# Optimization experiments

Hardware: AMD Instinct MI355X
Metric: run time of the kernel (lower is better)

## Reference

```python
import jax, jax.numpy as jnp
import numpy as np

N = 1_000_000   # total nodes (variable + check)
V = 600_000     # variable nodes (mask = first V nodes)
H = 128         # hidden_dim


def setup_inputs() -> dict:
    key = jax.random.key(0)
    k0, k1, k2, k3 = jax.random.split(key, 4)
    node_features = jax.random.normal(k0, (N, H), dtype=jnp.float32)
    original_llr = jax.random.normal(k1, (V,), dtype=jnp.float32)
    # canonical layout: variable nodes occupy the first V slots
    var_node_mask = jnp.arange(N) < V
    # llr_proj: Linear(1, H)
    W_llr = jax.random.normal(k2, (1, H), dtype=jnp.float32) * 0.1
    b_llr = jnp.zeros((H,), dtype=jnp.float32)
    # gate: Linear(2H, H) followed by sigmoid
    W_gate = jax.random.normal(k3, (2 * H, H), dtype=jnp.float32) * (1.0 / np.sqrt(2 * H))
    b_gate = jnp.zeros((H,), dtype=jnp.float32)
    return {
        "node_features": node_features,
        "original_llr": original_llr,
        "W_llr": W_llr,
        "b_llr": b_llr,
        "W_gate": W_gate,
        "b_gate": b_gate,
        "var_node_mask": var_node_mask,
    }


def reference(node_features, original_llr, W_llr, b_llr, W_gate, b_gate, var_node_mask):
    # var_node_mask is, by construction, True exactly for the first V nodes,
    # so the masked gather/scatter reduces to static slicing (jit-friendly).
    num_var = original_llr.shape[0]
    var_features = node_features[:num_var]                      # [V, H] gather
    # Linear(1 -> H): outer product of scalar llr with weight row + bias
    llr_features = original_llr[:, None] * W_llr[0] + b_llr      # [V, H]
    gate_in = jnp.concatenate([var_features, llr_features], axis=-1)  # [V, 2H]
    gate = jax.nn.sigmoid(gate_in @ W_gate + b_gate)             # [V, H]
    fused = gate * llr_features + (1.0 - gate) * var_features    # convex combo
    return node_features.at[:num_var].set(fused)                 # scatter back
```

## Files before the change

### kernel.cpp

```cpp
#include <hip/hip_runtime.h>
#include <hip/hip_bf16.h>

constexpr int H = 128;
constexpr int V = 600000;
constexpr int NTOT = 1000000;
constexpr int NT = 50;

typedef short bf16x8 __attribute__((ext_vector_type(8)));
typedef float f32x4 __attribute__((ext_vector_type(4)));
typedef unsigned int u32;

__device__ __forceinline__ short f2bf(float f) {
    unsigned u = __float_as_uint(f);
    u += 0x7FFF + ((u >> 16) & 1);
    return (short)(u >> 16);
}

__device__ __forceinline__ void async_copy16(char* ldsDst, const float* gSrc) {
    __builtin_amdgcn_global_load_lds(
        (const __attribute__((address_space(1))) u32*)gSrc,
        (__attribute__((address_space(3))) u32*)ldsDst, 16, 0, 0);
}
__device__ __forceinline__ void async_copy4(char* ldsDst, const float* gSrc) {
    __builtin_amdgcn_global_load_lds(
        (const __attribute__((address_space(1))) u32*)gSrc,
        (__attribute__((address_space(3))) u32*)ldsDst, 4, 0, 0);
}
#define FENCE() asm volatile("" ::: "memory")

__global__ void precompute_uc_kernel(const float* __restrict__ W_llr,
                                     const float* __restrict__ b_llr,
                                     const float* __restrict__ W_gate,
                                     const float* __restrict__ b_gate,
                                     float* __restrict__ uc) {
    int h = threadIdx.x;
    float u = 0.0f, c = 0.0f;
    for (int k = 0; k < H; ++k) {
        float w2 = W_gate[(size_t)(H + k) * H + h];
        u += W_llr[k] * w2;
        c += b_llr[k] * w2;
    }
    uc[h] = u;
    uc[H + h] = c + b_gate[h];
    uc[2 * H + h] = W_llr[h];
    uc[3 * H + h] = b_llr[h];
}

#define LDS_BYTES 32768
#define ABUF 8192
#define LLR_BASE 24576

__global__ __launch_bounds__(256, 4) void fused_residual_llr_kernel(
    const float* __restrict__ nf,
    const float* __restrict__ llr,
    const float* __restrict__ W_gate,
    const float* __restrict__ uc,
    float* __restrict__ out) {
    int b = blockIdx.x;
    int tid = threadIdx.x;

    if ((b & 3) == 3) {
        size_t base = (size_t)V * H;
        const float4* src = reinterpret_cast<const float4*>(nf + base);
        float4* dst = reinterpret_cast<float4*>(out + base);
        size_t i0 = (size_t)(b >> 2) * 256 + tid;
        const size_t stride = 250u * 256u;
#pragma unroll 1
        for (int s = 0; s < 50; ++s) {
            size_t i = i0 + (size_t)s * (stride * 4);
            float4 v0 = src[i];
            float4 v1 = src[i + stride];
            float4 v2 = src[i + 2 * stride];
            float4 v3 = src[i + 3 * stride];
            dst[i] = v0;
            dst[i + stride] = v1;
            dst[i + 2 * stride] = v2;
            dst[i + 3 * stride] = v3;
        }
        return;
    }
    int cb = (b >> 2) * 3 + (b & 3);

    __shared__ __align__(16) char lds[LDS_BYTES];

    int lane = tid & 63;
    int w = tid >> 6;
    int l15 = lane & 15;
    int l4 = lane >> 4;

#pragma unroll 4
    for (int j = 0; j < 16; ++j) {
        int idx = tid + 256 * j;
        int k = idx >> 5, c4 = idx & 31;
        float4 wv = reinterpret_cast<const float4*>(W_gate)[(size_t)k * 32 + c4];
        float wa[4] = {wv.x, wv.y, wv.z, wv.w};
#pragma unroll
        for (int e = 0; e < 4; ++e) {
            int n = c4 * 4 + e;
            *reinterpret_cast<short*>(lds + n * 256 + k * 2) = f2bf(wa[e]);
        }
    }
    float u_r[2], c_r[2], wl_r[2], bl_r[2];
#pragma unroll
    for (int nfr = 0; nfr < 2; ++nfr) {
        int col = w * 32 + nfr * 16 + l15;
        u_r[nfr]  = uc[col];
        c_r[nfr]  = uc[128 + col];
        wl_r[nfr] = uc[256 + col];
        bl_r[nfr] = uc[384 + col];
    }
    __syncthreads();

    bf16x8 Bf[4][2];
#pragma unroll
    for (int kk = 0; kk < 4; ++kk)
#pragma unroll
        for (int nfr = 0; nfr < 2; ++nfr) {
            int n = w * 32 + nfr * 16 + l15;
            Bf[kk][nfr] = *reinterpret_cast<const bf16x8*>(
                lds + n * 256 + kk * 64 + l4 * 16);
        }
    __syncthreads();

    int rowBase0 = cb * (NT * 16);

#define STAGE(tt, bi)                                                        \
    {                                                                        \
        char* nbuf_ = lds + (bi) * ABUF;                                     \
        int rb_ = rowBase0 + (tt) * 16;                                      \
        _Pragma("unroll")                                                    \
        for (int j_ = 0; j_ < 2; ++j_) {                                     \
            int seg_ = w * 2 + j_;                                           \
            int rl_ = seg_ * 2 + (lane >> 5);                                \
            int gg_ = (lane & 31) ^ (rl_ & 7);                               \
            async_copy16(nbuf_ + seg_ * 1024,                                \
                         nf + (size_t)(rb_ + rl_) * H + gg_ * 4);            \
        }                                                                    \
        async_copy4(lds + LLR_BASE + (bi) * 256, llr + rb_ + (lane & 15));   \
    }

    STAGE(0, 0);
    FENCE();
    STAGE(1, 1);
    FENCE();

    int cur = 0;
#pragma unroll 1
    for (int t = 0; t < NT; ++t) {
        int rowBase = rowBase0 + t * 16;

        if (t == NT - 1) asm volatile("s_waitcnt vmcnt(0)" ::: "memory");
        else             asm volatile("s_waitcnt vmcnt(3)" ::: "memory");
        __builtin_amdgcn_s_barrier();
        FENCE();

        if (t + 2 < NT) {
            int tgt = (cur == 0) ? 2 : cur - 1;
            STAGE(t + 2, tgt);
        }
        FENCE();

        char* buf = lds + cur * ABUF;
        f32x4 acc[2];
        acc[0] = (f32x4){0.f, 0.f, 0.f, 0.f};
        acc[1] = (f32x4){0.f, 0.f, 0.f, 0.f};
#pragma unroll
        for (int kk = 0; kk < 4; ++kk) {
            int g0 = (l4 * 2) ^ (l15 & 7);
            const char* base = buf + l15 * 512 + kk * 128;
            f32x4 lo = *reinterpret_cast<const f32x4*>(base + (g0 << 4));
            f32x4 hi = *reinterpret_cast<const f32x4*>(base + ((g0 ^ 1) << 4));
            bf16x8 a;
            a[0] = f2bf(lo[0]); a[1] = f2bf(lo[1]);
            a[2] = f2bf(lo[2]); a[3] = f2bf(lo[3]);
            a[4] = f2bf(hi[0]); a[5] = f2bf(hi[1]);
            a[6] = f2bf(hi[2]); a[7] = f2bf(hi[3]);
            acc[0] = __builtin_amdgcn_mfma_f32_16x16x32_bf16(
                a, Bf[kk][0], acc[0], 0, 0, 0);
            acc[1] = __builtin_amdgcn_mfma_f32_16x16x32_bf16(
                a, Bf[kk][1], acc[1], 0, 0, 0);
        }

        const float* llrs = reinterpret_cast<const float*>(lds + LLR_BASE + cur * 256);
#pragma unroll
        for (int reg = 0; reg < 4; ++reg) {
            int rl = l4 * 4 + reg;
            float lr = llrs[rl];
#pragma unroll
            for (int nfr = 0; nfr < 2; ++nfr) {
                int col = w * 32 + nfr * 16 + l15;
                float x = acc[nfr][reg] + fmaf(lr, u_r[nfr], c_r[nfr]);
                float g = 1.0f / (1.0f + __expf(-x));
                int gcol = w * 8 + nfr * 4 + (l15 >> 2);
                float vf = *reinterpret_cast<const float*>(
                    buf + rl * 512 + ((gcol ^ (rl & 7)) << 4) + (l15 & 3) * 4);
                float lf = fmaf(lr, wl_r[nfr], bl_r[nfr]);
                out[(size_t)(rowBase + rl) * H + col] = fmaf(g, lf - vf, vf);
            }
        }
        FENCE();
        cur = (cur == 2) ? 0 : cur + 1;
    }
}

extern "C" void kernel_launch(void* const* d_in, const int* in_sizes, int n_in,
                              void* d_out, int out_size, void* d_ws, size_t ws_size,
                              hipStream_t stream) {
    const float* nf     = (const float*)d_in[0];
    const float* llr    = (const float*)d_in[1];
    const float* W_llr  = (const float*)d_in[2];
    const float* b_llr  = (const float*)d_in[3];
    const float* W_gate = (const float*)d_in[4];
    const float* b_gate = (const float*)d_in[5];
    float* out = (float*)d_out;
    float* uc  = (float*)d_ws;

    precompute_uc_kernel<<<1, 128, 0, stream>>>(W_llr, b_llr, W_gate, b_gate, uc);

    fused_residual_llr_kernel<<<1000, 256, 0, stream>>>(nf, llr, W_gate, uc, out);
}
```

Measured before the change: 247.5 us.

## Use 32-row tiles, interleaved stripe assignment, and persistent 768-block grid

Doubles the row tile from 16 to 32 rows per iteration, so each wave issues two MFMA row groups and the LDS buffers grow to 16KB each with 3 blocks per CU. Rows are now handed out as interleaved stripes across 576 compute blocks, giving each block 32 or 33 tiles, and the grid shrinks to 768 blocks sized for roughly one wave of residency. The copy blocks move 8 float4 loads per iteration with bounds checks. The aim is to raise bytes in flight per block and cut per-tile overhead and tail imbalance. The cost is lower occupancy and hand-tuned vmcnt values that must match the new load counts exactly.

```diff
diff --git a/kernel.cpp b/kernel.cpp
--- a/kernel.cpp
+++ b/kernel.cpp
@@ -4,7 +4,8 @@
 constexpr int H = 128;
 constexpr int V = 600000;
 constexpr int NTOT = 1000000;
-constexpr int NT = 50;
+constexpr int NCB = 576;
+constexpr int NSTRIPE = 18750;
 
 typedef short bf16x8 __attribute__((ext_vector_type(8)));
 typedef float f32x4 __attribute__((ext_vector_type(4)));
@@ -46,11 +47,11 @@
     uc[3 * H + h] = b_llr[h];
 }
 
-#define LDS_BYTES 32768
-#define ABUF 8192
-#define LLR_BASE 24576
-
-__global__ __launch_bounds__(256, 4) void fused_residual_llr_kernel(
+#define LDS_BYTES 49920
+#define ABUF 16384
+#define LLR_BASE 49152
+
+__global__ __launch_bounds__(256, 3) void fused_residual_llr_kernel(
     const float* __restrict__ nf,
     const float* __restrict__ llr,
     const float* __restrict__ W_gate,
@@ -63,23 +64,28 @@
         size_t base = (size_t)V * H;
         const float4* src = reinterpret_cast<const float4*>(nf + base);
         float4* dst = reinterpret_cast<float4*>(out + base);
+        const size_t n4 = ((size_t)(NTOT - V) * H) / 4;
         size_t i0 = (size_t)(b >> 2) * 256 + tid;
-        const size_t stride = 250u * 256u;
+        const size_t stride = 192u * 256u;
 #pragma unroll 1
-        for (int s = 0; s < 50; ++s) {
-            size_t i = i0 + (size_t)s * (stride * 4);
-            float4 v0 = src[i];
-            float4 v1 = src[i + stride];
-            float4 v2 = src[i + 2 * stride];
-            float4 v3 = src[i + 3 * stride];
-            dst[i] = v0;
-            dst[i + stride] = v1;
-            dst[i + 2 * stride] = v2;
-            dst[i + 3 * stride] = v3;
+        for (int s = 0; s < 33; ++s) {
+            float4 v[8];
+            size_t ib = i0 + (size_t)(s * 8) * stride;
+#pragma unroll
+            for (int k = 0; k < 8; ++k) {
+                size_t i = ib + (size_t)k * stride;
+                if (i < n4) v[k] = src[i];
+            }
+#pragma unroll
+            for (int k = 0; k < 8; ++k) {
+                size_t i = ib + (size_t)k * stride;
+                if (i < n4) dst[i] = v[k];
+            }
         }
         return;
     }
     int cb = (b >> 2) * 3 + (b & 3);
+    int NTb = (cb < NSTRIPE - NCB * 32) ? 33 : 32;
 
     __shared__ __align__(16) char lds[LDS_BYTES];
 
@@ -122,21 +128,19 @@
         }
     __syncthreads();
 
-    int rowBase0 = cb * (NT * 16);
-
 #define STAGE(tt, bi)                                                        \
     {                                                                        \
         char* nbuf_ = lds + (bi) * ABUF;                                     \
-        int rb_ = rowBase0 + (tt) * 16;                                      \
+        int rb_ = (cb + NCB * (tt)) * 32;                                    \
         _Pragma("unroll")                                                    \
-        for (int j_ = 0; j_ < 2; ++j_) {                                     \
-            int seg_ = w * 2 + j_;                                           \
+        for (int j_ = 0; j_ < 4; ++j_) {                                     \
+            int seg_ = w * 4 + j_;                                           \
             int rl_ = seg_ * 2 + (lane >> 5);                                \
             int gg_ = (lane & 31) ^ (rl_ & 7);                               \
             async_copy16(nbuf_ + seg_ * 1024,                                \
                          nf + (size_t)(rb_ + rl_) * H + gg_ * 4);            \
         }                                                                    \
-        async_copy4(lds + LLR_BASE + (bi) * 256, llr + rb_ + (lane & 15));   \
+        async_copy4(lds + LLR_BASE + (bi) * 256, llr + rb_ + (lane & 31));   \
     }
 
     STAGE(0, 0);
@@ -146,56 +150,69 @@
 
     int cur = 0;
 #pragma unroll 1
-    for (int t = 0; t < NT; ++t) {
-        int rowBase = rowBase0 + t * 16;
-
-        if (t == NT - 1) asm volatile("s_waitcnt vmcnt(0)" ::: "memory");
-        else             asm volatile("s_waitcnt vmcnt(3)" ::: "memory");
+    for (int t = 0; t < NTb; ++t) {
+        int rowBase = (cb + NCB * t) * 32;
+
+        if (t == 0)            asm volatile("s_waitcnt vmcnt(5)" ::: "memory");
+        else if (t == 1)       asm volatile("s_waitcnt vmcnt(21)" ::: "memory");
+        else if (t == NTb - 1) asm volatile("s_waitcnt vmcnt(32)" ::: "memory");
+        else                   asm volatile("s_waitcnt vmcnt(37)" ::: "memory");
         __builtin_amdgcn_s_barrier();
         FENCE();
 
-        if (t + 2 < NT) {
+        if (t + 2 < NTb) {
             int tgt = (cur == 0) ? 2 : cur - 1;
             STAGE(t + 2, tgt);
         }
         FENCE();
 
         char* buf = lds + cur * ABUF;
-        f32x4 acc[2];
-        acc[0] = (f32x4){0.f, 0.f, 0.f, 0.f};
-        acc[1] = (f32x4){0.f, 0.f, 0.f, 0.f};
+        f32x4 acc[2][2];
+#pragma unroll
+        for (int mrg = 0; mrg < 2; ++mrg)
+#pragma unroll
+            for (int nfr = 0; nfr < 2; ++nfr)
+                acc[mrg][nfr] = (f32x4){0.f, 0.f, 0.f, 0.f};
+
 #pragma unroll
         for (int kk = 0; kk < 4; ++kk) {
             int g0 = (l4 * 2) ^ (l15 & 7);
-            const char* base = buf + l15 * 512 + kk * 128;
-            f32x4 lo = *reinterpret_cast<const f32x4*>(base + (g0 << 4));
-            f32x4 hi = *reinterpret_cast<const f32x4*>(base + ((g0 ^ 1) << 4));
-            bf16x8 a;
-            a[0] = f2bf(lo[0]); a[1] = f2bf(lo[1]);
-            a[2] = f2bf(lo[2]); a[3] = f2bf(lo[3]);
-            a[4] = f2bf(hi[0]); a[5] = f2bf(hi[1]);
-            a[6] = f2bf(hi[2]); a[7] = f2bf(hi[3]);
-            acc[0] = __builtin_amdgcn_mfma_f32_16x16x32_bf16(
-                a, Bf[kk][0], acc[0], 0, 0, 0);
-            acc[1] = __builtin_amdgcn_mfma_f32_16x16x32_bf16(
-                a, Bf[kk][1], acc[1], 0, 0, 0);
+#pragma unroll
+            for (int mrg = 0; mrg < 2; ++mrg) {
+                int rl = mrg * 16 + l15;
+                const char* base = buf + rl * 512 + kk * 128;
+                f32x4 lo = *reinterpret_cast<const f32x4*>(base + (g0 << 4));
+                f32x4 hi = *reinterpret_cast<const f32x4*>(base + ((g0 ^ 1) << 4));
+                bf16x8 a;
+                a[0] = f2bf(lo[0]); a[1] = f2bf(lo[1]);
+                a[2] = f2bf(lo[2]); a[3] = f2bf(lo[3]);
+                a[4] = f2bf(hi[0]); a[5] = f2bf(hi[1]);
+                a[6] = f2bf(hi[2]); a[7] = f2bf(hi[3]);
+                acc[mrg][0] = __builtin_amdgcn_mfma_f32_16x16x32_bf16(
+                    a, Bf[kk][0], acc[mrg][0], 0, 0, 0);
+                acc[mrg][1] = __builtin_amdgcn_mfma_f32_16x16x32_bf16(
+                    a, Bf[kk][1], acc[mrg][1], 0, 0, 0);
+            }
         }
 
         const float* llrs = reinterpret_cast<const float*>(lds + LLR_BASE + cur * 256);
 #pragma unroll
-        for (int reg = 0; reg < 4; ++reg) {
-            int rl = l4 * 4 + reg;
-            float lr = llrs[rl];
-#pragma unroll
-            for (int nfr = 0; nfr < 2; ++nfr) {
-                int col = w * 32 + nfr * 16 + l15;
-                float x = acc[nfr][reg] + fmaf(lr, u_r[nfr], c_r[nfr]);
-                float g = 1.0f / (1.0f + __expf(-x));
-                int gcol = w * 8 + nfr * 4 + (l15 >> 2);
-                float vf = *reinterpret_cast<const float*>(
-                    buf + rl * 512 + ((gcol ^ (rl & 7)) << 4) + (l15 & 3) * 4);
-                float lf = fmaf(lr, wl_r[nfr], bl_r[nfr]);
-                out[(size_t)(rowBase + rl) * H + col] = fmaf(g, lf - vf, vf);
+        for (int mrg = 0; mrg < 2; ++mrg) {
+#pragma unroll
+            for (int reg = 0; reg < 4; ++reg) {
+                int rl = mrg * 16 + l4 * 4 + reg;
+                float lr = llrs[rl];
+#pragma unroll
+                for (int nfr = 0; nfr < 2; ++nfr) {
+                    int col = w * 32 + nfr * 16 + l15;
+                    float x = acc[mrg][nfr][reg] + fmaf(lr, u_r[nfr], c_r[nfr]);
+                    float g = 1.0f / (1.0f + __expf(-x));
+                    int gcol = w * 8 + nfr * 4 + (l15 >> 2);
+                    float vf = *reinterpret_cast<const float*>(
+                        buf + rl * 512 + ((gcol ^ (rl & 7)) << 4) + (l15 & 3) * 4);
+                    float lf = fmaf(lr, wl_r[nfr], bl_r[nfr]);
+                    out[(size_t)(rowBase + rl) * H + col] = fmaf(g, lf - vf, vf);
+                }
             }
         }
         FENCE();
@@ -217,5 +234,5 @@
 
     precompute_uc_kernel<<<1, 128, 0, stream>>>(W_llr, b_llr, W_gate, b_gate, uc);
 
-    fused_residual_llr_kernel<<<1000, 256, 0, stream>>>(nf, llr, W_gate, uc, out);
-}
+    fused_residual_llr_kernel<<<768, 256, 0, stream>>>(nf, llr, W_gate, uc, out);
+}
```

After: 411.9 us. 66.4% more time.
